# Performance work log

Hardware: AMD Instinct MI355X
Metric: run time of the kernel (lower is better)

The kernel has to match this reference:

```python
import jax, jax.numpy as jnp
import numpy as np

A, N, D, H, ADIM = 8, 32768, 128, 4, 32  # agents, batch, hidden, heads, attend_dim


def setup_inputs() -> dict:
    key = jax.random.key(0)
    ks = jax.random.split(key, 7)
    querys = jax.random.normal(ks[0], (A, N, D), jnp.float32)
    keys = jax.random.normal(ks[1], (A, N, D), jnp.float32)
    values = jax.random.normal(ks[2], (A, N, D), jnp.float32)
    s = 1.0 / np.sqrt(D)
    Wk = jax.random.normal(ks[3], (H, ADIM, D), jnp.float32) * s   # key_extractors (no bias)
    Wsel = jax.random.normal(ks[4], (H, ADIM, D), jnp.float32) * s  # selector_extractors (no bias)
    Wv = jax.random.normal(ks[5], (H, ADIM, D), jnp.float32) * s   # value_extractors Linear
    bv = jax.random.normal(ks[6], (H, ADIM), jnp.float32) * s      # value_extractors bias
    return {"querys": querys, "keys": keys, "values": values,
            "Wk": Wk, "Wsel": Wsel, "Wv": Wv, "bv": bv}


def _offdiag_idx(a):
    # idx[i, j] enumerates the a-1 agents != i, in order (matches torch list comp j != a_i)
    j = jnp.arange(a - 1)[None, :]
    i = jnp.arange(a)[:, None]
    return jnp.where(j < i, j, j + 1)  # [A, A-1]


def reference(querys, keys, values, Wk, Wsel, Wv, bv):
    # per-head projections: [H, A, N, K]
    hk = jnp.einsum('and,hkd->hank', keys, Wk)
    hs = jnp.einsum('and,hkd->hank', querys, Wsel)
    hv = jax.nn.leaky_relu(jnp.einsum('and,hkd->hank', values, Wv) + bv[:, None, None, :],
                           negative_slope=0.01)
    # full logits over all key-agents j for each query-agent i: [H, A, N, A]
    logits_full = jnp.einsum('hink,hjnk->hinj', hs, hk)
    scale = 1.0 / jnp.sqrt(jnp.asarray(hk.shape[-1], hk.dtype))
    # self-exclusion: mask j == i so softmax over j equals softmax over the other agents
    self_mask = jnp.eye(A, dtype=bool)[None, :, None, :]
    probs_full = jax.nn.softmax(jnp.where(self_mask, -1e9, logits_full * scale), axis=-1)
    # attended values: [H, A, N, K] (diagonal prob is exactly 0 after masking? it is ~e^{-1e9} ~ 0)
    other = jnp.einsum('hinj,hjnk->hink', probs_full, hv)
    # gather the self-excluded logits/probs in the original (A-1)-length layout
    idx = _offdiag_idx(A)
    idx4 = jnp.broadcast_to(idx[None, :, None, :], logits_full.shape[:-1] + (A - 1,))
    logits_ex = jnp.take_along_axis(logits_full, idx4, axis=-1)  # [H, A, N, A-1]
    probs_ex = jnp.take_along_axis(probs_full, idx4, axis=-1)    # [H, A, N, A-1]
    # reorder to agent-major like the torch nested lists: [A, H, ...]
    return (jnp.swapaxes(other, 0, 1),
            jnp.swapaxes(logits_ex, 0, 1),
            jnp.swapaxes(probs_ex, 0, 1))
```

## Files before the change

kernel.cpp:

```cpp
#include <hip/hip_runtime.h>
#include <hip/hip_bf16.h>

typedef unsigned short u16;
typedef unsigned int u32;

#define AGT 8
#define NBATCH 32768
#define DDIM 128
#define HEADS 4
#define KDIM 32
#define CC 128
#define NT 8
#define MROWS 64

typedef float f32x4 __attribute__((ext_vector_type(4)));
typedef __bf16 bf16x8 __attribute__((ext_vector_type(8)));
typedef short s16x8 __attribute__((ext_vector_type(8)));

union FragU { s16x8 s; bf16x8 b; };

__device__ __forceinline__ u16 f2bf(float f) {
  u32 u = __float_as_uint(f);
  u = (u + 0x7FFFu + ((u >> 16) & 1u)) >> 16;
  return (u16)u;
}
__device__ __forceinline__ float bf2f(u16 u) {
  return __uint_as_float(((u32)u) << 16);
}

__global__ void prep_weights(const float* __restrict__ Wk,
                             const float* __restrict__ Ws,
                             const float* __restrict__ Wv,
                             u16* __restrict__ Wb) {
  int idx = blockIdx.x * 256 + threadIdx.x;
  if (idx >= 3 * 8 * 4 * 64 * 8) return;
  int b  = idx & 7;
  int l  = (idx >> 3) & 63;
  int kc = (idx >> 9) & 3;
  int ct = (idx >> 11) & 7;
  int pj = idx >> 14;
  int c = ct * 16 + (l & 15);
  int h = c >> 5, kk = c & 31;
  int d = kc * 32 + ((b >> 2) << 4) + ((l >> 4) << 2) + (b & 3);
  const float* W = (pj == 0) ? Wk : ((pj == 1) ? Ws : Wv);
  Wb[idx] = f2bf(W[(h * KDIM + kk) * DDIM + d]);
}

__global__ __launch_bounds__(256, 3) void fused_attn(
    const float* __restrict__ qin, const float* __restrict__ kin,
    const float* __restrict__ vin, const u16* __restrict__ Wb,
    const float* __restrict__ bv,
    float* __restrict__ out0, float* __restrict__ out1,
    float* __restrict__ out2) {
  __shared__ __align__(16) u16 sH[3][MROWS * CC];

  const int tid = threadIdx.x;
  const int l = tid & 63;
  const int w = tid >> 6;
  const int n0 = blockIdx.x * NT;
  const int lr = l & 15;
  const int lg = l >> 4;

  const int arow = w * 16 + lr;
  const size_t grow_off =
      ((size_t)(arow >> 3) * NBATCH + (size_t)(n0 + (arow & 7))) * DDIM;

#pragma unroll
  for (int pj = 0; pj < 3; ++pj) {
    const float* X = (pj == 0) ? kin : ((pj == 1) ? qin : vin);
    const float* grow = X + grow_off;

    FragU fa[4];
#pragma unroll
    for (int kc = 0; kc < 4; ++kc) {
      const float4 x0 = *(const float4*)(grow + kc * 32 + lg * 4);
      const float4 x1 = *(const float4*)(grow + kc * 32 + lg * 4 + 16);
      s16x8 t;
      t[0] = (short)f2bf(x0.x); t[1] = (short)f2bf(x0.y);
      t[2] = (short)f2bf(x0.z); t[3] = (short)f2bf(x0.w);
      t[4] = (short)f2bf(x1.x); t[5] = (short)f2bf(x1.y);
      t[6] = (short)f2bf(x1.z); t[7] = (short)f2bf(x1.w);
      fa[kc].s = t;
    }

    f32x4 acc[8];
#pragma unroll
    for (int ct = 0; ct < 8; ++ct) acc[ct] = (f32x4)(0.0f);

#pragma unroll
    for (int ct = 0; ct < 8; ++ct) {
#pragma unroll
      for (int kc = 0; kc < 4; ++kc) {
        FragU fb;
        fb.s = *(const s16x8*)(Wb + ((((pj * 8 + ct) * 4 + kc) * 64 + l) << 3));
        acc[ct] = __builtin_amdgcn_mfma_f32_16x16x32_bf16(fa[kc].b, fb.b,
                                                          acc[ct], 0, 0, 0);
      }
    }

    u16* dst = sH[pj];
#pragma unroll
    for (int ct = 0; ct < 8; ++ct) {
      const int c = ct * 16 + lr;
      float bias = 0.0f;
      if (pj == 2) bias = bv[c];
#pragma unroll
      for (int rg = 0; rg < 4; ++rg) {
        const int row = w * 16 + lg * 4 + rg;
        float x = acc[ct][rg];
        if (pj == 2) { x += bias; x = (x > 0.0f) ? x : 0.01f * x; }
        const int off = row * 256 + ((c * 2) ^ ((row & 7) << 4));
        *(u16*)((char*)dst + off) = f2bf(x);
      }
    }
  }

  __syncthreads();

  const int h = w;
  const int i = l >> 3;
  const int nt = l & 7;
  const int n = n0 + nt;
  const int cb2 = h * 64;

  float hsv[32];
  {
    const int r = i * 8 + nt;
    const int swz = (r & 7) << 4;
#pragma unroll
    for (int qc = 0; qc < 4; ++qc) {
      s16x8 ch = *(const s16x8*)((const char*)sH[1] + r * 256 +
                                 ((cb2 + qc * 16) ^ swz));
#pragma unroll
      for (int e = 0; e < 8; ++e) hsv[qc * 8 + e] = bf2f((u16)(u32)(int)ch[e] & 0xFFFFu);
    }
  }

  float logits[8];
#pragma unroll
  for (int j = 0; j < 8; ++j) {
    const int r = j * 8 + nt;
    const int swz = (r & 7) << 4;
    float a = 0.0f;
#pragma unroll
    for (int qc = 0; qc < 4; ++qc) {
      s16x8 ch = *(const s16x8*)((const char*)sH[0] + r * 256 +
                                 ((cb2 + qc * 16) ^ swz));
#pragma unroll
      for (int e = 0; e < 8; ++e)
        a = fmaf(hsv[qc * 8 + e], bf2f((u16)(u32)(int)ch[e] & 0xFFFFu), a);
    }
    logits[j] = a;
  }

  const float scale = 0.17677669529663687f;
  float sl[8];
#pragma unroll
  for (int j = 0; j < 8; ++j) sl[j] = (j == i) ? -1e30f : logits[j] * scale;
  float m = sl[0];
#pragma unroll
  for (int j = 1; j < 8; ++j) m = fmaxf(m, sl[j]);
  float p[8];
  float s = 0.0f;
#pragma unroll
  for (int j = 0; j < 8; ++j) { p[j] = __expf(sl[j] - m); s += p[j]; }
  const float inv = 1.0f / s;

  const size_t ob = ((size_t)(i * HEADS + h) * NBATCH + (size_t)n);
  const size_t ob7 = ob * 7;
#pragma unroll
  for (int j = 0; j < 8; ++j) {
    if (j != i) {
      const int jj = j - ((j > i) ? 1 : 0);
      out1[ob7 + jj] = logits[j];
      out2[ob7 + jj] = p[j] * inv;
    }
  }

  float oacc[32];
#pragma unroll
  for (int e = 0; e < 32; ++e) oacc[e] = 0.0f;
#pragma unroll
  for (int j = 0; j < 8; ++j) {
    const float pw = p[j] * inv;
    const int r = j * 8 + nt;
    const int swz = (r & 7) << 4;
#pragma unroll
    for (int qc = 0; qc < 4; ++qc) {
      s16x8 ch = *(const s16x8*)((const char*)sH[2] + r * 256 +
                                 ((cb2 + qc * 16) ^ swz));
#pragma unroll
      for (int e = 0; e < 8; ++e)
        oacc[qc * 8 + e] = fmaf(pw, bf2f((u16)(u32)(int)ch[e] & 0xFFFFu),
                                oacc[qc * 8 + e]);
    }
  }

  const size_t o0 = ob * 32;
#pragma unroll
  for (int qc = 0; qc < 8; ++qc) {
    float4 vv = make_float4(oacc[qc * 4 + 0], oacc[qc * 4 + 1],
                            oacc[qc * 4 + 2], oacc[qc * 4 + 3]);
    *(float4*)(out0 + o0 + qc * 4) = vv;
  }
}

extern "C" void kernel_launch(void* const* d_in, const int* in_sizes, int n_in,
                              void* d_out, int out_size, void* d_ws,
                              size_t ws_size, hipStream_t stream) {
  const float* qin = (const float*)d_in[0];
  const float* kin = (const float*)d_in[1];
  const float* vin = (const float*)d_in[2];
  const float* Wk  = (const float*)d_in[3];
  const float* Ws  = (const float*)d_in[4];
  const float* Wv  = (const float*)d_in[5];
  const float* bvp = (const float*)d_in[6];

  float* out0 = (float*)d_out;
  float* out1 = out0 + (size_t)AGT * HEADS * NBATCH * KDIM;
  float* out2 = out1 + (size_t)AGT * HEADS * NBATCH * 7;

  u16* Wb = (u16*)d_ws;

  prep_weights<<<dim3(192), dim3(256), 0, stream>>>(Wk, Ws, Wv, Wb);
  fused_attn<<<dim3(NBATCH / NT), dim3(256), 0, stream>>>(
      qin, kin, vin, Wb, bvp, out0, out1, out2);
}
```

Before: 232.1 us.

## Keep projections in registers and compute attention logits and outputs with MFMA

Removes the shared-memory staging of projected K/Q/V. Each wave now handles 2 batch rows times 8 agents as a 16-row MFMA tile, computes transposed projections so the results land directly in MFMA operand layout, and uses MFMA for both the QK logits and the P·V product. The softmax uses cross-lane shuffles, with masking for self-agent and mismatched batch parity. This trades LDS traffic and the block barrier for wasted MFMA work (half the logit tile is masked, half of each K operand is zero-padded) and for scattered 4-byte output stores that replace float4 stores.

```diff
diff --git a/kernel.cpp b/kernel.cpp
--- a/kernel.cpp
+++ b/kernel.cpp
@@ -9,23 +9,22 @@
 #define DDIM 128
 #define HEADS 4
 #define KDIM 32
-#define CC 128
-#define NT 8
-#define MROWS 64
 
 typedef float f32x4 __attribute__((ext_vector_type(4)));
 typedef __bf16 bf16x8 __attribute__((ext_vector_type(8)));
 typedef short s16x8 __attribute__((ext_vector_type(8)));
-
-union FragU { s16x8 s; bf16x8 b; };
+typedef u32 u32x4 __attribute__((ext_vector_type(4)));
+
+union FragU { s16x8 s; bf16x8 b; u32x4 u; };
 
 __device__ __forceinline__ u16 f2bf(float f) {
   u32 u = __float_as_uint(f);
   u = (u + 0x7FFFu + ((u >> 16) & 1u)) >> 16;
   return (u16)u;
 }
-__device__ __forceinline__ float bf2f(u16 u) {
-  return __uint_as_float(((u32)u) << 16);
+
+__device__ __forceinline__ u32 packbf(float lo, float hi) {
+  return (u32)f2bf(lo) | ((u32)f2bf(hi) << 16);
 }
 
 __global__ void prep_weights(const float* __restrict__ Wk,
@@ -37,171 +36,199 @@
   int b  = idx & 7;
   int l  = (idx >> 3) & 63;
   int kc = (idx >> 9) & 3;
-  int ct = (idx >> 11) & 7;
+  int t  = (idx >> 11) & 7;
   int pj = idx >> 14;
-  int c = ct * 16 + (l & 15);
+  int c = t * 16 + (l & 15);
   int h = c >> 5, kk = c & 31;
   int d = kc * 32 + ((b >> 2) << 4) + ((l >> 4) << 2) + (b & 3);
   const float* W = (pj == 0) ? Wk : ((pj == 1) ? Ws : Wv);
   Wb[idx] = f2bf(W[(h * KDIM + kk) * DDIM + d]);
 }
 
-__global__ __launch_bounds__(256, 3) void fused_attn(
+__device__ __forceinline__ void load_pack_row(const float* __restrict__ rowp,
+                                              int lg, FragU f[4]) {
+#pragma unroll
+  for (int kc = 0; kc < 4; ++kc) {
+    const float4 x0 = *(const float4*)(rowp + kc * 32 + lg * 4);
+    const float4 x1 = *(const float4*)(rowp + kc * 32 + lg * 4 + 16);
+    u32x4 t;
+    t[0] = packbf(x0.x, x0.y);
+    t[1] = packbf(x0.z, x0.w);
+    t[2] = packbf(x1.x, x1.y);
+    t[3] = packbf(x1.z, x1.w);
+    f[kc].u = t;
+  }
+}
+
+__global__ __launch_bounds__(256, 2) void fused_attn(
     const float* __restrict__ qin, const float* __restrict__ kin,
     const float* __restrict__ vin, const u16* __restrict__ Wb,
     const float* __restrict__ bv,
     float* __restrict__ out0, float* __restrict__ out1,
     float* __restrict__ out2) {
-  __shared__ __align__(16) u16 sH[3][MROWS * CC];
-
   const int tid = threadIdx.x;
   const int l = tid & 63;
   const int w = tid >> 6;
-  const int n0 = blockIdx.x * NT;
   const int lr = l & 15;
   const int lg = l >> 4;
-
-  const int arow = w * 16 + lr;
-  const size_t grow_off =
-      ((size_t)(arow >> 3) * NBATCH + (size_t)(n0 + (arow & 7))) * DDIM;
-
-#pragma unroll
-  for (int pj = 0; pj < 3; ++pj) {
-    const float* X = (pj == 0) ? kin : ((pj == 1) ? qin : vin);
-    const float* grow = X + grow_off;
-
-    FragU fa[4];
-#pragma unroll
-    for (int kc = 0; kc < 4; ++kc) {
-      const float4 x0 = *(const float4*)(grow + kc * 32 + lg * 4);
-      const float4 x1 = *(const float4*)(grow + kc * 32 + lg * 4 + 16);
-      s16x8 t;
-      t[0] = (short)f2bf(x0.x); t[1] = (short)f2bf(x0.y);
-      t[2] = (short)f2bf(x0.z); t[3] = (short)f2bf(x0.w);
-      t[4] = (short)f2bf(x1.x); t[5] = (short)f2bf(x1.y);
-      t[6] = (short)f2bf(x1.z); t[7] = (short)f2bf(x1.w);
-      fa[kc].s = t;
-    }
-
-    f32x4 acc[8];
-#pragma unroll
-    for (int ct = 0; ct < 8; ++ct) acc[ct] = (f32x4)(0.0f);
-
-#pragma unroll
-    for (int ct = 0; ct < 8; ++ct) {
+  const int n_base = blockIdx.x * 8 + w * 2;
+  const int my_agent = lr >> 1;
+  const int my_n = n_base + (lr & 1);
+  const size_t xoff = ((size_t)my_agent * NBATCH + (size_t)my_n) * DDIM;
+
+  const f32x4 zero4 = (f32x4)(0.0f);
+
+  FragU hk4[HEADS];
+  {
+    FragU fx[4];
+    load_pack_row(kin + xoff, lg, fx);
+    f32x4 a[8];
+#pragma unroll
+    for (int mt = 0; mt < 8; ++mt) {
+      a[mt] = zero4;
 #pragma unroll
       for (int kc = 0; kc < 4; ++kc) {
         FragU fb;
-        fb.s = *(const s16x8*)(Wb + ((((pj * 8 + ct) * 4 + kc) * 64 + l) << 3));
-        acc[ct] = __builtin_amdgcn_mfma_f32_16x16x32_bf16(fa[kc].b, fb.b,
-                                                          acc[ct], 0, 0, 0);
-      }
-    }
-
-    u16* dst = sH[pj];
+        fb.s = *(const s16x8*)(Wb + ((((0 * 8 + mt) * 4 + kc) * 64 + l) << 3));
+        a[mt] = __builtin_amdgcn_mfma_f32_16x16x32_bf16(fb.b, fx[kc].b, a[mt],
+                                                        0, 0, 0);
+      }
+    }
+#pragma unroll
+    for (int h = 0; h < HEADS; ++h) {
+      u32x4 t;
+      t[0] = packbf(a[2 * h][0], a[2 * h][1]);
+      t[1] = packbf(a[2 * h][2], a[2 * h][3]);
+      t[2] = packbf(a[2 * h + 1][0], a[2 * h + 1][1]);
+      t[3] = packbf(a[2 * h + 1][2], a[2 * h + 1][3]);
+      hk4[h].u = t;
+    }
+  }
+
+  FragU hs4[HEADS];
+  {
+    FragU fx[4];
+    load_pack_row(qin + xoff, lg, fx);
+    f32x4 a[8];
+#pragma unroll
+    for (int mt = 0; mt < 8; ++mt) {
+      a[mt] = zero4;
+#pragma unroll
+      for (int kc = 0; kc < 4; ++kc) {
+        FragU fb;
+        fb.s = *(const s16x8*)(Wb + ((((1 * 8 + mt) * 4 + kc) * 64 + l) << 3));
+        a[mt] = __builtin_amdgcn_mfma_f32_16x16x32_bf16(fb.b, fx[kc].b, a[mt],
+                                                        0, 0, 0);
+      }
+    }
+#pragma unroll
+    for (int h = 0; h < HEADS; ++h) {
+      u32x4 t;
+      t[0] = packbf(a[2 * h][0], a[2 * h][1]);
+      t[1] = packbf(a[2 * h][2], a[2 * h][3]);
+      t[2] = packbf(a[2 * h + 1][0], a[2 * h + 1][1]);
+      t[3] = packbf(a[2 * h + 1][2], a[2 * h + 1][3]);
+      hs4[h].u = t;
+    }
+  }
+
+  FragU hv4[8];
+  {
+    FragU fx[4];
+    load_pack_row(vin + xoff, lg, fx);
 #pragma unroll
     for (int ct = 0; ct < 8; ++ct) {
-      const int c = ct * 16 + lr;
-      float bias = 0.0f;
-      if (pj == 2) bias = bv[c];
+      f32x4 a = zero4;
+#pragma unroll
+      for (int kc = 0; kc < 4; ++kc) {
+        FragU fb;
+        fb.s = *(const s16x8*)(Wb + ((((2 * 8 + ct) * 4 + kc) * 64 + l) << 3));
+        a = __builtin_amdgcn_mfma_f32_16x16x32_bf16(fx[kc].b, fb.b, a, 0, 0, 0);
+      }
+      const float bias = bv[ct * 16 + lr];
+      float x[4];
 #pragma unroll
       for (int rg = 0; rg < 4; ++rg) {
-        const int row = w * 16 + lg * 4 + rg;
-        float x = acc[ct][rg];
-        if (pj == 2) { x += bias; x = (x > 0.0f) ? x : 0.01f * x; }
-        const int off = row * 256 + ((c * 2) ^ ((row & 7) << 4));
-        *(u16*)((char*)dst + off) = f2bf(x);
-      }
-    }
-  }
-
-  __syncthreads();
-
-  const int h = w;
-  const int i = l >> 3;
-  const int nt = l & 7;
-  const int n = n0 + nt;
-  const int cb2 = h * 64;
-
-  float hsv[32];
-  {
-    const int r = i * 8 + nt;
-    const int swz = (r & 7) << 4;
-#pragma unroll
-    for (int qc = 0; qc < 4; ++qc) {
-      s16x8 ch = *(const s16x8*)((const char*)sH[1] + r * 256 +
-                                 ((cb2 + qc * 16) ^ swz));
-#pragma unroll
-      for (int e = 0; e < 8; ++e) hsv[qc * 8 + e] = bf2f((u16)(u32)(int)ch[e] & 0xFFFFu);
-    }
-  }
-
-  float logits[8];
-#pragma unroll
-  for (int j = 0; j < 8; ++j) {
-    const int r = j * 8 + nt;
-    const int swz = (r & 7) << 4;
-    float a = 0.0f;
-#pragma unroll
-    for (int qc = 0; qc < 4; ++qc) {
-      s16x8 ch = *(const s16x8*)((const char*)sH[0] + r * 256 +
-                                 ((cb2 + qc * 16) ^ swz));
-#pragma unroll
-      for (int e = 0; e < 8; ++e)
-        a = fmaf(hsv[qc * 8 + e], bf2f((u16)(u32)(int)ch[e] & 0xFFFFu), a);
-    }
-    logits[j] = a;
+        float v = a[rg] + bias;
+        x[rg] = (v > 0.0f) ? v : 0.01f * v;
+      }
+      u32x4 t;
+      t[0] = packbf(x[0], x[1]);
+      t[1] = packbf(x[2], x[3]);
+      t[2] = 0;
+      t[3] = 0;
+      hv4[ct].u = t;
+    }
   }
 
   const float scale = 0.17677669529663687f;
-  float sl[8];
-#pragma unroll
-  for (int j = 0; j < 8; ++j) sl[j] = (j == i) ? -1e30f : logits[j] * scale;
-  float m = sl[0];
-#pragma unroll
-  for (int j = 1; j < 8; ++j) m = fmaxf(m, sl[j]);
-  float p[8];
-  float s = 0.0f;
-#pragma unroll
-  for (int j = 0; j < 8; ++j) { p[j] = __expf(sl[j] - m); s += p[j]; }
-  const float inv = 1.0f / s;
-
-  const size_t ob = ((size_t)(i * HEADS + h) * NBATCH + (size_t)n);
-  const size_t ob7 = ob * 7;
-#pragma unroll
-  for (int j = 0; j < 8; ++j) {
-    if (j != i) {
-      const int jj = j - ((j > i) ? 1 : 0);
-      out1[ob7 + jj] = logits[j];
-      out2[ob7 + jj] = p[j] * inv;
-    }
-  }
-
-  float oacc[32];
-#pragma unroll
-  for (int e = 0; e < 32; ++e) oacc[e] = 0.0f;
-#pragma unroll
-  for (int j = 0; j < 8; ++j) {
-    const float pw = p[j] * inv;
-    const int r = j * 8 + nt;
-    const int swz = (r & 7) << 4;
-#pragma unroll
-    for (int qc = 0; qc < 4; ++qc) {
-      s16x8 ch = *(const s16x8*)((const char*)sH[2] + r * 256 +
-                                 ((cb2 + qc * 16) ^ swz));
-#pragma unroll
-      for (int e = 0; e < 8; ++e)
-        oacc[qc * 8 + e] = fmaf(pw, bf2f((u16)(u32)(int)ch[e] & 0xFFFFu),
-                                oacc[qc * 8 + e]);
-    }
-  }
-
-  const size_t o0 = ob * 32;
-#pragma unroll
-  for (int qc = 0; qc < 8; ++qc) {
-    float4 vv = make_float4(oacc[qc * 4 + 0], oacc[qc * 4 + 1],
-                            oacc[qc * 4 + 2], oacc[qc * 4 + 3]);
-    *(float4*)(out0 + o0 + qc * 4) = vv;
+  const int ipar = lr & 1;
+
+#pragma unroll
+  for (int h = 0; h < HEADS; ++h) {
+    f32x4 S = __builtin_amdgcn_mfma_f32_16x16x32_bf16(hk4[h].b, hs4[h].b,
+                                                      zero4, 0, 0, 0);
+    float sl[4];
+#pragma unroll
+    for (int rg = 0; rg < 4; ++rg) {
+      const int jrow = 4 * lg + rg;
+      const bool valid = ((rg & 1) == ipar) && (jrow != lr);
+      sl[rg] = valid ? S[rg] * scale : -1e30f;
+    }
+    float mp = fmaxf(fmaxf(sl[0], sl[1]), fmaxf(sl[2], sl[3]));
+    mp = fmaxf(mp, __shfl_xor(mp, 16));
+    mp = fmaxf(mp, __shfl_xor(mp, 32));
+    float e[4];
+    float sp = 0.0f;
+#pragma unroll
+    for (int rg = 0; rg < 4; ++rg) {
+      e[rg] = __expf(sl[rg] - mp);
+      sp += e[rg];
+    }
+    sp += __shfl_xor(sp, 16);
+    sp += __shfl_xor(sp, 32);
+    const float inv = 1.0f / sp;
+    float p[4];
+#pragma unroll
+    for (int rg = 0; rg < 4; ++rg) p[rg] = e[rg] * inv;
+
+    const int a_i = lr >> 1;
+    const int n = n_base + ipar;
+    const size_t ob7 = ((size_t)(a_i * HEADS + h) * NBATCH + (size_t)n) * 7;
+#pragma unroll
+    for (int rg = 0; rg < 4; ++rg) {
+      const int jrow = 4 * lg + rg;
+      if (((rg & 1) == ipar) && (jrow != lr)) {
+        const int a_j = jrow >> 1;
+        const int jj = a_j - ((a_j > a_i) ? 1 : 0);
+        out1[ob7 + jj] = S[rg];
+        out2[ob7 + jj] = p[rg];
+      }
+    }
+
+    FragU P;
+    {
+      u32x4 t;
+      t[0] = packbf(p[0], p[1]);
+      t[1] = packbf(p[2], p[3]);
+      t[2] = 0;
+      t[3] = 0;
+      P.u = t;
+    }
+    f32x4 O0 = __builtin_amdgcn_mfma_f32_16x16x32_bf16(P.b, hv4[2 * h].b,
+                                                       zero4, 0, 0, 0);
+    f32x4 O1 = __builtin_amdgcn_mfma_f32_16x16x32_bf16(P.b, hv4[2 * h + 1].b,
+                                                       zero4, 0, 0, 0);
+#pragma unroll
+    for (int rg = 0; rg < 4; ++rg) {
+      const int irow = 4 * lg + rg;
+      const int a_o = irow >> 1;
+      const int n_o = n_base + (irow & 1);
+      const size_t o0 =
+          ((size_t)(a_o * HEADS + h) * NBATCH + (size_t)n_o) * KDIM;
+      out0[o0 + lr] = O0[rg];
+      out0[o0 + 16 + lr] = O1[rg];
+    }
   }
 }
 
@@ -223,6 +250,6 @@
   u16* Wb = (u16*)d_ws;
 
   prep_weights<<<dim3(192), dim3(256), 0, stream>>>(Wk, Ws, Wv, Wb);
-  fused_attn<<<dim3(NBATCH / NT), dim3(256), 0, stream>>>(
+  fused_attn<<<dim3(NBATCH / 8), dim3(256), 0, stream>>>(
       qin, kin, vin, Wb, bvp, out0, out1, out2);
 }
```

Measured after the change: 272.0 us. 1.17x slower.
